# Optimization experiments

Hardware: AMD Instinct MI355X
Metric: run time of the kernel (lower is better)

## Reference

```python
import jax, jax.numpy as jnp
import numpy as np

NUM_HEADS = 8


def _mha(x, w_in, b_in, w_out, b_out, nh=NUM_HEADS):
    # x: [B, L, H]; torch nn.MultiheadAttention (batch_first) self-attention
    B, L, H = x.shape
    dh = H // nh
    qkv = x @ w_in.T + b_in                      # [B, L, 3H]
    q, k, v = jnp.split(qkv, 3, axis=-1)
    def heads(t):
        return t.reshape(B, L, nh, dh).transpose(0, 2, 1, 3)  # [B, nh, L, dh]
    q, k, v = heads(q), heads(k), heads(v)
    scale = 1.0 / np.sqrt(dh)
    scores = jnp.einsum('bhqd,bhkd->bhqk', q * scale, k)      # [B, nh, L, L]
    attn = jax.nn.softmax(scores, axis=-1)
    out = jnp.einsum('bhqk,bhkd->bhqd', attn, v)               # [B, nh, L, dh]
    out = out.transpose(0, 2, 1, 3).reshape(B, L, H)
    return out @ w_out.T + b_out


def setup_inputs() -> dict:
    key = jax.random.key(0)
    ks = jax.random.split(key, 10)
    S, M, B, H = 64, 4, 128, 1024
    std = 0.02
    inp = {
        'hidden_states_combined': jax.random.normal(ks[0], (S, M, B, 1, H), jnp.float32),
        'mf_in_w': jax.random.normal(ks[1], (3 * H, H), jnp.float32) * std,
        'mf_in_b': jnp.zeros((3 * H,), jnp.float32),
        'mf_out_w': jax.random.normal(ks[2], (H, H), jnp.float32) * std,
        'mf_out_b': jnp.zeros((H,), jnp.float32),
        'sf_in_w': jax.random.normal(ks[3], (3 * H, H), jnp.float32) * std,
        'sf_in_b': jnp.zeros((3 * H,), jnp.float32),
        'sf_out_w': jax.random.normal(ks[4], (H, H), jnp.float32) * std,
        'sf_out_b': jnp.zeros((H,), jnp.float32),
        'pos_enc': jax.random.normal(ks[5], (1, S, H), jnp.float32) * std,
    }
    return inp


def reference(hidden_states_combined, mf_in_w, mf_in_b, mf_out_w, mf_out_b,
              sf_in_w, sf_in_b, sf_out_w, sf_out_b, pos_enc):
    S, M, B, _, H = hidden_states_combined.shape
    # [S, M, B, 1, H] -> [S, B, M, H] -> batch all steps together: [S*B, M, H]
    x = hidden_states_combined[:, :, :, 0, :].transpose(0, 2, 1, 3).reshape(S * B, M, H)
    fused = _mha(x, mf_in_w, mf_in_b, mf_out_w, mf_out_b)        # [S*B, M, H]
    fused = fused.mean(axis=1).reshape(S, B, H)                  # mean over models
    seq = fused.transpose(1, 0, 2) + pos_enc[:, :S, :]            # [B, S, H]
    enhanced = _mha(seq, sf_in_w, sf_in_b, sf_out_w, sf_out_b)   # [B, S, H]
    return enhanced.transpose(1, 0, 2)[:, :, None, :]             # [S, B, 1, H]
```

## Files before the change

### kernel.cpp

```cpp
#include <hip/hip_runtime.h>

typedef unsigned short u16;
typedef __attribute__((ext_vector_type(8))) short bf16x8;
typedef __attribute__((ext_vector_type(4))) float f32x4;

__device__ __forceinline__ u16 f2bf(float f) {
  unsigned u = __float_as_uint(f);
  u += 0x7FFFu + ((u >> 16) & 1u);
  return (u16)(u >> 16);
}
__device__ __forceinline__ float bf2f(u16 h) {
  return __uint_as_float(((unsigned)h) << 16);
}

#define GLOAD16(g, l) __builtin_amdgcn_global_load_lds( \
    (const __attribute__((address_space(1))) void*)(g), \
    (__attribute__((address_space(3))) void*)(l), 16, 0, 0)

__global__ __launch_bounds__(256) void cvtw_kernel(const float* __restrict__ in,
                                                   u16* __restrict__ out, int n4) {
  int i = blockIdx.x * 256 + threadIdx.x;
  if (i >= n4) return;
  float4 f = ((const float4*)in)[i];
  ushort4 u;
  u.x = f2bf(f.x); u.y = f2bf(f.y); u.z = f2bf(f.z); u.w = f2bf(f.w);
  ((ushort4*)out)[i] = u;
}

__global__ __launch_bounds__(256) void xcvt_kernel(const float* __restrict__ hidden,
                                                   u16* __restrict__ xb, int s0) {
  int idx = blockIdx.x * 256 + threadIdx.x;
  int h4 = idx & 255;
  int lrow = idx >> 8;
  int m = lrow & 3;
  int b = (lrow >> 2) & 127;
  int sl = lrow >> 9;
  int s = s0 + sl;
  const float4 f = *(const float4*)(hidden + (((size_t)(s * 4 + m) * 128 + b) * 1024) + h4 * 4);
  ushort4 u;
  u.x = f2bf(f.x); u.y = f2bf(f.y); u.z = f2bf(f.z); u.w = f2bf(f.w);
  *(ushort4*)(xb + (size_t)lrow * 1024 + h4 * 4) = u;
}

template <int MODE>
__global__ __launch_bounds__(256) void gemm_bt(const u16* __restrict__ A,
                                               const u16* __restrict__ Bw,
                                               const float* __restrict__ bias,
                                               void* __restrict__ Cout,
                                               int M, int N, int K,
                                               const float* __restrict__ posenc) {
  __shared__ u16 As[128 * 32];
  __shared__ u16 Bs[128 * 32];
  const int t = threadIdx.x;
  const int w = t >> 6, l = t & 63;
  const int rowBase = blockIdx.y * 128, colBase = blockIdx.x * 128;
  const int wr = (w >> 1) * 64, wc = (w & 1) * 64;
  const int lr = l & 15, lg = l >> 4;
  const int sl = (lg ^ (lr & 3)) * 8;

  const int r0 = t >> 2,         s0 = (((t) & 3) ^ (r0 & 3)) * 8;
  const int r1 = (t + 256) >> 2, s1 = (((t + 256) & 3) ^ (r1 & 3)) * 8;
  const u16* A0 = A + (size_t)(rowBase + r0) * K + s0;
  const u16* A1 = A + (size_t)(rowBase + r1) * K + s1;
  const u16* B0 = Bw + (size_t)(colBase + r0) * K + s0;
  const u16* B1 = Bw + (size_t)(colBase + r1) * K + s1;
  u16* lA0 = As + (w * 64) * 8;
  u16* lA1 = As + (256 + w * 64) * 8;
  u16* lB0 = Bs + (w * 64) * 8;
  u16* lB1 = Bs + (256 + w * 64) * 8;

  f32x4 acc[4][4];
#pragma unroll
  for (int i = 0; i < 4; i++)
#pragma unroll
    for (int j = 0; j < 4; j++) acc[i][j] = (f32x4){0.f, 0.f, 0.f, 0.f};

  for (int k0 = 0; k0 < K; k0 += 32) {
    GLOAD16(A0 + k0, lA0);
    GLOAD16(A1 + k0, lA1);
    GLOAD16(B0 + k0, lB0);
    GLOAD16(B1 + k0, lB1);
    __syncthreads();
    bf16x8 af[4], bfv[4];
#pragma unroll
    for (int i = 0; i < 4; i++) af[i] = *(const bf16x8*)(As + (wr + i * 16 + lr) * 32 + sl);
#pragma unroll
    for (int j = 0; j < 4; j++) bfv[j] = *(const bf16x8*)(Bs + (wc + j * 16 + lr) * 32 + sl);
#pragma unroll
    for (int i = 0; i < 4; i++)
#pragma unroll
      for (int j = 0; j < 4; j++)
        acc[i][j] = __builtin_amdgcn_mfma_f32_16x16x32_bf16(af[i], bfv[j], acc[i][j], 0, 0, 0);
    __syncthreads();
  }

  const int orow0 = rowBase + wr + lg * 4;
  const int ocol0 = colBase + wc + lr;
#pragma unroll
  for (int i = 0; i < 4; i++) {
#pragma unroll
    for (int j = 0; j < 4; j++) {
#pragma unroll
      for (int r = 0; r < 4; r++) {
        int row = orow0 + i * 16 + r;
        int col = ocol0 + j * 16;
        float v = acc[i][j][r] + bias[col];
        if (MODE == 0) {
          ((u16*)Cout)[(size_t)row * N + col] = f2bf(v);
        } else if (MODE == 1) {
          int s = row >> 7, b = row & 127;
          v += posenc[s * 1024 + col];
          ((u16*)Cout)[((size_t)(b * 64 + s)) * 1024 + col] = f2bf(v);
        } else {
          int s = row & 63, b = row >> 6;
          ((float*)Cout)[((size_t)(s * 128 + b)) * 1024 + col] = v;
        }
      }
    }
  }
}

__global__ __launch_bounds__(256) void attn1_kernel(const u16* __restrict__ qkv,
                                                    u16* __restrict__ am, int seqBase) {
  const int w = threadIdx.x >> 6, l = threadIdx.x & 63;
  const int pair = blockIdx.x * 4 + w;
  const int seq = pair >> 3, head = pair & 7;
  const int d0 = l * 2;
  const u16* base = qkv + (size_t)(seq * 4) * 3072 + head * 128 + d0;
  const float scale = 0.08838834764831845f;
  float q[4][2], k[4][2], v[4][2];
#pragma unroll
  for (int m = 0; m < 4; m++) {
    ushort2 uq = *(const ushort2*)(base + (size_t)m * 3072);
    ushort2 uk = *(const ushort2*)(base + (size_t)m * 3072 + 1024);
    ushort2 uv = *(const ushort2*)(base + (size_t)m * 3072 + 2048);
    q[m][0] = bf2f(uq.x) * scale; q[m][1] = bf2f(uq.y) * scale;
    k[m][0] = bf2f(uk.x);         k[m][1] = bf2f(uk.y);
    v[m][0] = bf2f(uv.x);         v[m][1] = bf2f(uv.y);
  }
  float sc[4][4];
#pragma unroll
  for (int i = 0; i < 4; i++)
#pragma unroll
    for (int j = 0; j < 4; j++)
      sc[i][j] = q[i][0] * k[j][0] + q[i][1] * k[j][1];
#pragma unroll
  for (int off = 32; off >= 1; off >>= 1)
#pragma unroll
    for (int i = 0; i < 4; i++)
#pragma unroll
      for (int j = 0; j < 4; j++)
        sc[i][j] += __shfl_xor(sc[i][j], off, 64);
  float pbar[4] = {0.f, 0.f, 0.f, 0.f};
#pragma unroll
  for (int i = 0; i < 4; i++) {
    float mx = fmaxf(fmaxf(sc[i][0], sc[i][1]), fmaxf(sc[i][2], sc[i][3]));
    float e0 = __expf(sc[i][0] - mx), e1 = __expf(sc[i][1] - mx);
    float e2 = __expf(sc[i][2] - mx), e3 = __expf(sc[i][3] - mx);
    float inv = 0.25f / (e0 + e1 + e2 + e3);
    pbar[0] += e0 * inv; pbar[1] += e1 * inv; pbar[2] += e2 * inv; pbar[3] += e3 * inv;
  }
  float o0 = pbar[0] * v[0][0] + pbar[1] * v[1][0] + pbar[2] * v[2][0] + pbar[3] * v[3][0];
  float o1 = pbar[0] * v[0][1] + pbar[1] * v[1][1] + pbar[2] * v[2][1] + pbar[3] * v[3][1];
  ushort2 ou; ou.x = f2bf(o0); ou.y = f2bf(o1);
  *(ushort2*)(am + (size_t)(seqBase + seq) * 1024 + head * 128 + d0) = ou;
}

__global__ __launch_bounds__(256) void attn2_kernel(const u16* __restrict__ qkv2,
                                                    u16* __restrict__ aout) {
  __shared__ u16 Qs[64 * 128];
  __shared__ u16 Ks[64 * 128];
  __shared__ u16 Vt[128 * 72];
  __shared__ u16 Ps[64 * 72];
  const int t = threadIdx.x, w = t >> 6, l = t & 63;
  const int lr = l & 15, lg = l >> 4;
  const int b = blockIdx.x >> 3, head = blockIdx.x & 7;
  const u16* qb = qkv2 + (size_t)(b * 64) * 3072 + head * 128;

#pragma unroll
  for (int c = 0; c < 4; c++) {
    int flat = c * 256 + t;
    int row = flat >> 4, sp = flat & 15;
    int sg = (sp ^ (row & 7)) * 8;
    GLOAD16(qb + (size_t)row * 3072 + sg, Qs + (c * 256 + w * 64) * 8);
    GLOAD16(qb + 1024 + (size_t)row * 3072 + sg, Ks + (c * 256 + w * 64) * 8);
  }
  const int dd = (t & 63) * 2, kb = t >> 6;
#pragma unroll
  for (int c = 0; c < 16; c++) {
    int k = c * 4 + kb;
    ushort2 vv = *(const ushort2*)(qb + 2048 + (size_t)k * 3072 + dd);
    Vt[(size_t)dd * 72 + k] = vv.x;
    Vt[(size_t)(dd + 1) * 72 + k] = vv.y;
  }
  __syncthreads();

  f32x4 sc[4];
#pragma unroll
  for (int cb = 0; cb < 4; cb++) sc[cb] = (f32x4){0.f, 0.f, 0.f, 0.f};
#pragma unroll
  for (int ks = 0; ks < 4; ks++) {
    bf16x8 aq = *(const bf16x8*)(Qs + (w * 16 + lr) * 128 + ((ks * 4 + lg) ^ (lr & 7)) * 8);
#pragma unroll
    for (int cb = 0; cb < 4; cb++) {
      bf16x8 bk = *(const bf16x8*)(Ks + (cb * 16 + lr) * 128 + ((ks * 4 + lg) ^ (lr & 7)) * 8);
      sc[cb] = __builtin_amdgcn_mfma_f32_16x16x32_bf16(aq, bk, sc[cb], 0, 0, 0);
    }
  }

  const float scale = 0.08838834764831845f;
#pragma unroll
  for (int r = 0; r < 4; r++) {
#pragma unroll
    for (int cb = 0; cb < 4; cb++) sc[cb][r] *= scale;
    float mx = fmaxf(fmaxf(sc[0][r], sc[1][r]), fmaxf(sc[2][r], sc[3][r]));
#pragma unroll
    for (int off = 1; off < 16; off <<= 1) mx = fmaxf(mx, __shfl_xor(mx, off, 64));
    float sum = 0.f;
#pragma unroll
    for (int cb = 0; cb < 4; cb++) {
      float e = __expf(sc[cb][r] - mx);
      sum += e;
      sc[cb][r] = e;
    }
#pragma unroll
    for (int off = 1; off < 16; off <<= 1) sum += __shfl_xor(sum, off, 64);
    float inv = 1.f / sum;
    int prow = w * 16 + lg * 4 + r;
#pragma unroll
    for (int cb = 0; cb < 4; cb++)
      Ps[(size_t)prow * 72 + cb * 16 + lr] = f2bf(sc[cb][r] * inv);
  }

  f32x4 o[8];
#pragma unroll
  for (int cb = 0; cb < 8; cb++) o[cb] = (f32x4){0.f, 0.f, 0.f, 0.f};
#pragma unroll
  for (int ks = 0; ks < 2; ks++) {
    bf16x8 ap = *(const bf16x8*)(Ps + (w * 16 + lr) * 72 + ks * 32 + lg * 8);
#pragma unroll
    for (int cb = 0; cb < 8; cb++) {
      bf16x8 bv = *(const bf16x8*)(Vt + (cb * 16 + lr) * 72 + ks * 32 + lg * 8);
      o[cb] = __builtin_amdgcn_mfma_f32_16x16x32_bf16(ap, bv, o[cb], 0, 0, 0);
    }
  }
#pragma unroll
  for (int cb = 0; cb < 8; cb++) {
#pragma unroll
    for (int r = 0; r < 4; r++) {
      int srow = w * 16 + lg * 4 + r;
      int d = cb * 16 + lr;
      aout[(size_t)(b * 64 + srow) * 1024 + head * 128 + d] = f2bf(o[cb][r]);
    }
  }
}

extern "C" void kernel_launch(void* const* d_in, const int* in_sizes, int n_in,
                              void* d_out, int out_size, void* d_ws, size_t ws_size,
                              hipStream_t stream) {
  const float* hidden   = (const float*)d_in[0];
  const float* mf_in_w  = (const float*)d_in[1];
  const float* mf_in_b  = (const float*)d_in[2];
  const float* mf_out_w = (const float*)d_in[3];
  const float* mf_out_b = (const float*)d_in[4];
  const float* sf_in_w  = (const float*)d_in[5];
  const float* sf_in_b  = (const float*)d_in[6];
  const float* sf_out_w = (const float*)d_in[7];
  const float* sf_out_b = (const float*)d_in[8];
  const float* pos_enc  = (const float*)d_in[9];

  char* ws = (char*)d_ws;
  u16* w_mf_in  = (u16*)(ws);
  u16* w_mf_out = (u16*)(ws + 6291456);
  u16* w_sf_in  = (u16*)(ws + 8388608);
  u16* w_sf_out = (u16*)(ws + 14680064);
  u16* xchunk   = (u16*)(ws + 16777216);
  u16* qkvbuf   = (u16*)(ws + 33554432);
  u16* attnmean = (u16*)(ws + 83886080);
  u16* seqbuf   = (u16*)(ws + 100663296);
  u16* a2out    = (u16*)(ws + 117440512);

  cvtw_kernel<<<3072, 256, 0, stream>>>(mf_in_w, w_mf_in, 786432);
  cvtw_kernel<<<1024, 256, 0, stream>>>(mf_out_w, w_mf_out, 262144);
  cvtw_kernel<<<3072, 256, 0, stream>>>(sf_in_w, w_sf_in, 786432);
  cvtw_kernel<<<1024, 256, 0, stream>>>(sf_out_w, w_sf_out, 262144);

  for (int c = 0; c < 4; ++c) {
    xcvt_kernel<<<8192, 256, 0, stream>>>(hidden, xchunk, c * 16);
    gemm_bt<0><<<dim3(24, 64), 256, 0, stream>>>(xchunk, w_mf_in, mf_in_b, qkvbuf,
                                                 8192, 3072, 1024, nullptr);
    attn1_kernel<<<4096, 256, 0, stream>>>(qkvbuf, attnmean, c * 2048);
  }

  gemm_bt<1><<<dim3(8, 64), 256, 0, stream>>>(attnmean, w_mf_out, mf_out_b, seqbuf,
                                              8192, 1024, 1024, pos_enc);
  gemm_bt<0><<<dim3(24, 64), 256, 0, stream>>>(seqbuf, w_sf_in, sf_in_b, qkvbuf,
                                               8192, 3072, 1024, nullptr);
  attn2_kernel<<<1024, 256, 0, stream>>>(qkvbuf, a2out);
  gemm_bt<2><<<dim3(8, 64), 256, 0, stream>>>(a2out, w_sf_out, sf_out_b, d_out,
                                              8192, 1024, 1024, nullptr);
}
```

Baseline: 573.8 us.

## Add 256x256 triple-buffered bf16 GEMM for QKV in-projections

Adds a new GEMM kernel with 256x256 output tiles, 512 threads, and a three-stage LDS ring fed by async global-to-LDS loads. It uses explicit vmcnt waits so the loads for tile k+2 overlap the MFMA work on tile k, and it raises wave priority around the MFMA block. Both in-projection GEMMs (8192x3072x1024) now use it. The larger tile gives more reuse per loaded byte, at the cost of higher register and LDS pressure (96KB LDS, 128 accumulator floats per lane) and a grid of only 384 blocks.

```diff
diff --git a/kernel.cpp b/kernel.cpp
--- a/kernel.cpp
+++ b/kernel.cpp
@@ -40,6 +40,95 @@
   ushort4 u;
   u.x = f2bf(f.x); u.y = f2bf(f.y); u.z = f2bf(f.z); u.w = f2bf(f.w);
   *(ushort4*)(xb + (size_t)lrow * 1024 + h4 * 4) = u;
+}
+
+__global__ __launch_bounds__(512, 2) void gemm256(const u16* __restrict__ A,
+                                                  const u16* __restrict__ Bw,
+                                                  const float* __restrict__ bias,
+                                                  u16* __restrict__ C,
+                                                  int N, int K) {
+  __shared__ u16 SA[3][8192];
+  __shared__ u16 SB[3][8192];
+  const int t = threadIdx.x, w = t >> 6, l = t & 63;
+  const int lr = l & 15, lg = l >> 4;
+  const int wm = w >> 2, wn = w & 3;
+  const int rowBase = blockIdx.y * 256, colBase = blockIdx.x * 256;
+
+  const int srow = l >> 2;
+  const int gsl = ((l & 3) ^ (srow & 3)) * 8;
+  const u16* Ag0 = A + (size_t)(rowBase + w * 16 + srow) * K + gsl;
+  const u16* Ag1 = Ag0 + (size_t)128 * K;
+  const u16* Bg0 = Bw + (size_t)(colBase + w * 16 + srow) * K + gsl;
+  const u16* Bg1 = Bg0 + (size_t)128 * K;
+
+  const int fsl = (lg ^ (lr & 3)) * 8;
+  const int aoffB = (wm * 128 + lr) * 32 + fsl;
+  const int boffB = (wn * 64 + lr) * 32 + fsl;
+
+  f32x4 acc[8][4];
+#pragma unroll
+  for (int i = 0; i < 8; i++)
+#pragma unroll
+    for (int j = 0; j < 4; j++) acc[i][j] = (f32x4){0.f, 0.f, 0.f, 0.f};
+
+#define STG(tt, bb) do { \
+    const int k0_ = (tt) * 32; \
+    GLOAD16(Ag0 + k0_, &SA[bb][w * 512]); \
+    GLOAD16(Ag1 + k0_, &SA[bb][4096 + w * 512]); \
+    GLOAD16(Bg0 + k0_, &SB[bb][w * 512]); \
+    GLOAD16(Bg1 + k0_, &SB[bb][4096 + w * 512]); \
+  } while (0)
+
+  const int nt = K >> 5;
+  STG(0, 0);
+  STG(1, 1);
+  asm volatile("s_waitcnt vmcnt(4)" ::: "memory");
+  __builtin_amdgcn_s_barrier();
+  asm volatile("" ::: "memory");
+
+  int b0 = 0, b1 = 1, b2 = 2;
+  for (int tile = 0; tile < nt; ++tile) {
+    if (tile + 2 < nt) STG(tile + 2, b2);
+    const u16* pa = SA[b0];
+    const u16* pb = SB[b0];
+    bf16x8 af[8], bfr[4];
+#pragma unroll
+    for (int i = 0; i < 8; i++) af[i] = *(const bf16x8*)(pa + aoffB + i * 512);
+#pragma unroll
+    for (int j = 0; j < 4; j++) bfr[j] = *(const bf16x8*)(pb + boffB + j * 512);
+    __builtin_amdgcn_s_setprio(1);
+#pragma unroll
+    for (int i = 0; i < 8; i++)
+#pragma unroll
+      for (int j = 0; j < 4; j++)
+        acc[i][j] = __builtin_amdgcn_mfma_f32_16x16x32_bf16(af[i], bfr[j], acc[i][j], 0, 0, 0);
+    __builtin_amdgcn_s_setprio(0);
+    if (tile + 2 < nt) {
+      asm volatile("s_waitcnt vmcnt(4)" ::: "memory");
+    } else {
+      asm volatile("s_waitcnt vmcnt(0)" ::: "memory");
+    }
+    __builtin_amdgcn_s_barrier();
+    asm volatile("" ::: "memory");
+    const int tmp = b0; b0 = b1; b1 = b2; b2 = tmp;
+  }
+#undef STG
+
+  const int orow0 = rowBase + wm * 128 + lg * 4;
+  const int ocol0 = colBase + wn * 64 + lr;
+#pragma unroll
+  for (int i = 0; i < 8; i++) {
+#pragma unroll
+    for (int j = 0; j < 4; j++) {
+      const int col = ocol0 + j * 16;
+      const float bv = bias[col];
+#pragma unroll
+      for (int r = 0; r < 4; r++) {
+        const int row = orow0 + i * 16 + r;
+        C[(size_t)row * N + col] = f2bf(acc[i][j][r] + bv);
+      }
+    }
+  }
 }
 
 template <int MODE>
@@ -105,9 +194,7 @@
         int row = orow0 + i * 16 + r;
         int col = ocol0 + j * 16;
         float v = acc[i][j][r] + bias[col];
-        if (MODE == 0) {
-          ((u16*)Cout)[(size_t)row * N + col] = f2bf(v);
-        } else if (MODE == 1) {
+        if (MODE == 1) {
           int s = row >> 7, b = row & 127;
           v += posenc[s * 1024 + col];
           ((u16*)Cout)[((size_t)(b * 64 + s)) * 1024 + col] = f2bf(v);
@@ -287,15 +374,15 @@
 
   for (int c = 0; c < 4; ++c) {
     xcvt_kernel<<<8192, 256, 0, stream>>>(hidden, xchunk, c * 16);
-    gemm_bt<0><<<dim3(24, 64), 256, 0, stream>>>(xchunk, w_mf_in, mf_in_b, qkvbuf,
-                                                 8192, 3072, 1024, nullptr);
+    gemm256<<<dim3(12, 32), 512, 0, stream>>>(xchunk, w_mf_in, mf_in_b, qkvbuf,
+                                              3072, 1024);
     attn1_kernel<<<4096, 256, 0, stream>>>(qkvbuf, attnmean, c * 2048);
   }
 
   gemm_bt<1><<<dim3(8, 64), 256, 0, stream>>>(attnmean, w_mf_out, mf_out_b, seqbuf,
                                               8192, 1024, 1024, pos_enc);
-  gemm_bt<0><<<dim3(24, 64), 256, 0, stream>>>(seqbuf, w_sf_in, sf_in_b, qkvbuf,
-                                               8192, 3072, 1024, nullptr);
+  gemm256<<<dim3(12, 32), 512, 0, stream>>>(seqbuf, w_sf_in, sf_in_b, qkvbuf,
+                                            3072, 1024);
   attn2_kernel<<<1024, 256, 0, stream>>>(qkvbuf, a2out);
   gemm_bt<2><<<dim3(8, 64), 256, 0, stream>>>(a2out, w_sf_out, sf_out_b, d_out,
                                               8192, 1024, 1024, nullptr);
```

New measurement: 640.6 us. 1.12x slower.

## Replace GEMM with triple-buffered 256x128 tile pipeline and block swizzle

Applied to the files above, without the earlier changes.

Replaces the single-buffered 128x128 bf16 GEMM with a 256x128 tile kernel that uses three LDS stages. Global-to-LDS loads for tile k+2 are issued while MFMAs run on tile k, using split load phases, explicit waitcnt, barriers and setprio. A block-index remap groups neighbouring tiles to improve L2 reuse. This removes the per-iteration load/sync stalls of the old kernel, at the cost of more LDS (72KB), more registers and a grid half as large.

```diff
diff --git a/kernel.cpp b/kernel.cpp
--- a/kernel.cpp
+++ b/kernel.cpp
@@ -43,68 +43,120 @@
 }
 
 template <int MODE>
-__global__ __launch_bounds__(256) void gemm_bt(const u16* __restrict__ A,
-                                               const u16* __restrict__ Bw,
-                                               const float* __restrict__ bias,
-                                               void* __restrict__ Cout,
-                                               int M, int N, int K,
-                                               const float* __restrict__ posenc) {
-  __shared__ u16 As[128 * 32];
-  __shared__ u16 Bs[128 * 32];
-  const int t = threadIdx.x;
-  const int w = t >> 6, l = t & 63;
-  const int rowBase = blockIdx.y * 128, colBase = blockIdx.x * 128;
-  const int wr = (w >> 1) * 64, wc = (w & 1) * 64;
+__global__ __launch_bounds__(256, 2) void gemm_fp(const u16* __restrict__ A,
+                                                  const u16* __restrict__ Bw,
+                                                  const float* __restrict__ bias,
+                                                  void* __restrict__ Cout,
+                                                  int N, int K,
+                                                  const float* __restrict__ posenc) {
+  __shared__ u16 SA[3][8192];
+  __shared__ u16 SB[3][4096];
+  const int t = threadIdx.x, w = t >> 6, l = t & 63;
   const int lr = l & 15, lg = l >> 4;
-  const int sl = (lg ^ (lr & 3)) * 8;
-
-  const int r0 = t >> 2,         s0 = (((t) & 3) ^ (r0 & 3)) * 8;
-  const int r1 = (t + 256) >> 2, s1 = (((t + 256) & 3) ^ (r1 & 3)) * 8;
-  const u16* A0 = A + (size_t)(rowBase + r0) * K + s0;
-  const u16* A1 = A + (size_t)(rowBase + r1) * K + s1;
-  const u16* B0 = Bw + (size_t)(colBase + r0) * K + s0;
-  const u16* B1 = Bw + (size_t)(colBase + r1) * K + s1;
-  u16* lA0 = As + (w * 64) * 8;
-  u16* lA1 = As + (256 + w * 64) * 8;
-  u16* lB0 = Bs + (w * 64) * 8;
-  u16* lB1 = Bs + (256 + w * 64) * 8;
-
-  f32x4 acc[4][4];
-#pragma unroll
-  for (int i = 0; i < 4; i++)
+  const int wm = w >> 1, wn = w & 1;
+
+  const int gx = gridDim.x;
+  const int nb = gx * gridDim.y;
+  const int id = blockIdx.y * gx + blockIdx.x;
+  const int id2 = (id & 7) * (nb >> 3) + (id >> 3);
+  const int rowBase = (id2 / gx) * 256, colBase = (id2 % gx) * 128;
+
+  const int srow = l >> 2;
+  const int ssl = ((l & 3) ^ (srow & 3)) * 8;
+  const u16* Ag = A + (size_t)(rowBase + w * 16 + srow) * K + ssl;
+  const u16* Bg = Bw + (size_t)(colBase + w * 16 + srow) * K + ssl;
+  u16* const lA = &SA[0][0] + w * 512;
+  u16* const lB = &SB[0][0] + w * 512;
+
+  const int fsw = (lg ^ (lr & 3)) * 8;
+  const int aoff = (wm * 128 + lr) * 32 + fsw;
+  const int boff = (wn * 64 + lr) * 32 + fsw;
+
+  f32x4 acc[8][4];
+#pragma unroll
+  for (int i = 0; i < 8; i++)
 #pragma unroll
     for (int j = 0; j < 4; j++) acc[i][j] = (f32x4){0.f, 0.f, 0.f, 0.f};
 
-  for (int k0 = 0; k0 < K; k0 += 32) {
-    GLOAD16(A0 + k0, lA0);
-    GLOAD16(A1 + k0, lA1);
-    GLOAD16(B0 + k0, lB0);
-    GLOAD16(B1 + k0, lB1);
-    __syncthreads();
-    bf16x8 af[4], bfv[4];
-#pragma unroll
-    for (int i = 0; i < 4; i++) af[i] = *(const bf16x8*)(As + (wr + i * 16 + lr) * 32 + sl);
-#pragma unroll
-    for (int j = 0; j < 4; j++) bfv[j] = *(const bf16x8*)(Bs + (wc + j * 16 + lr) * 32 + sl);
-#pragma unroll
-    for (int i = 0; i < 4; i++)
-#pragma unroll
-      for (int j = 0; j < 4; j++)
-        acc[i][j] = __builtin_amdgcn_mfma_f32_16x16x32_bf16(af[i], bfv[j], acc[i][j], 0, 0, 0);
-    __syncthreads();
-  }
-
-  const int orow0 = rowBase + wr + lg * 4;
-  const int ocol0 = colBase + wc + lr;
-#pragma unroll
-  for (int i = 0; i < 4; i++) {
-#pragma unroll
-    for (int j = 0; j < 4; j++) {
+#define STG_P0(tt, bb) do { \
+    const size_t ko_ = (size_t)(tt) * 32; \
+    GLOAD16(Ag + ko_,                    lA + (bb) * 8192); \
+    GLOAD16(Ag + ko_ + (size_t)64 * K,   lA + (bb) * 8192 + 2048); \
+    GLOAD16(Ag + ko_ + (size_t)128 * K,  lA + (bb) * 8192 + 4096); \
+  } while (0)
+#define STG_P1(tt, bb) do { \
+    const size_t ko_ = (size_t)(tt) * 32; \
+    GLOAD16(Ag + ko_ + (size_t)192 * K,  lA + (bb) * 8192 + 6144); \
+    GLOAD16(Bg + ko_,                    lB + (bb) * 4096); \
+    GLOAD16(Bg + ko_ + (size_t)64 * K,   lB + (bb) * 4096 + 2048); \
+  } while (0)
+
+  const int nt = K >> 5;
+  STG_P0(0, 0); STG_P1(0, 0);
+  STG_P0(1, 1); STG_P1(1, 1);
+  asm volatile("s_waitcnt vmcnt(6)" ::: "memory");
+  __builtin_amdgcn_s_barrier();
+
+  int bcur = 0;
+  for (int tt = 0; tt < nt; ++tt) {
+    const u16* pa = &SA[bcur][0];
+    const u16* pb = &SB[bcur][0];
+    const int bnext = (bcur + 2 > 2) ? bcur - 1 : bcur + 2;
+    bf16x8 af[4], bfr[4];
+
+#pragma unroll
+    for (int m = 0; m < 4; m++) af[m] = *(const bf16x8*)(pa + aoff + m * 512);
+#pragma unroll
+    for (int n = 0; n < 4; n++) bfr[n] = *(const bf16x8*)(pb + boff + n * 512);
+    if (tt + 2 < nt) STG_P0(tt + 2, bnext);
+    __builtin_amdgcn_s_barrier();
+    asm volatile("s_waitcnt lgkmcnt(0)" ::: "memory");
+    __builtin_amdgcn_sched_barrier(0);
+    __builtin_amdgcn_s_setprio(1);
+#pragma unroll
+    for (int m = 0; m < 4; m++)
+#pragma unroll
+      for (int n = 0; n < 4; n++)
+        acc[m][n] = __builtin_amdgcn_mfma_f32_16x16x32_bf16(af[m], bfr[n], acc[m][n], 0, 0, 0);
+    __builtin_amdgcn_s_setprio(0);
+    __builtin_amdgcn_s_barrier();
+
+#pragma unroll
+    for (int m = 0; m < 4; m++) af[m] = *(const bf16x8*)(pa + aoff + (m + 4) * 512);
+    if (tt + 2 < nt) STG_P1(tt + 2, bnext);
+    __builtin_amdgcn_s_barrier();
+    asm volatile("s_waitcnt lgkmcnt(0)" ::: "memory");
+    __builtin_amdgcn_sched_barrier(0);
+    __builtin_amdgcn_s_setprio(1);
+#pragma unroll
+    for (int m = 0; m < 4; m++)
+#pragma unroll
+      for (int n = 0; n < 4; n++)
+        acc[m + 4][n] = __builtin_amdgcn_mfma_f32_16x16x32_bf16(af[m], bfr[n], acc[m + 4][n], 0, 0, 0);
+    __builtin_amdgcn_s_setprio(0);
+    if (tt + 2 < nt) {
+      asm volatile("s_waitcnt vmcnt(6)" ::: "memory");
+    } else if (tt + 1 < nt) {
+      asm volatile("s_waitcnt vmcnt(0)" ::: "memory");
+    }
+    __builtin_amdgcn_s_barrier();
+    bcur = (bcur + 1 > 2) ? 0 : bcur + 1;
+  }
+#undef STG_P0
+#undef STG_P1
+
+  const int orow0 = rowBase + wm * 128 + lg * 4;
+  const int ocol0 = colBase + wn * 64 + lr;
+#pragma unroll
+  for (int m = 0; m < 8; m++) {
+#pragma unroll
+    for (int n = 0; n < 4; n++) {
+      const int col = ocol0 + n * 16;
+      const float bv = bias[col];
 #pragma unroll
       for (int r = 0; r < 4; r++) {
-        int row = orow0 + i * 16 + r;
-        int col = ocol0 + j * 16;
-        float v = acc[i][j][r] + bias[col];
+        const int row = orow0 + m * 16 + r;
+        float v = acc[m][n][r] + bv;
         if (MODE == 0) {
           ((u16*)Cout)[(size_t)row * N + col] = f2bf(v);
         } else if (MODE == 1) {
@@ -287,16 +339,16 @@
 
   for (int c = 0; c < 4; ++c) {
     xcvt_kernel<<<8192, 256, 0, stream>>>(hidden, xchunk, c * 16);
-    gemm_bt<0><<<dim3(24, 64), 256, 0, stream>>>(xchunk, w_mf_in, mf_in_b, qkvbuf,
-                                                 8192, 3072, 1024, nullptr);
+    gemm_fp<0><<<dim3(24, 32), 256, 0, stream>>>(xchunk, w_mf_in, mf_in_b, qkvbuf,
+                                                 3072, 1024, nullptr);
     attn1_kernel<<<4096, 256, 0, stream>>>(qkvbuf, attnmean, c * 2048);
   }
 
-  gemm_bt<1><<<dim3(8, 64), 256, 0, stream>>>(attnmean, w_mf_out, mf_out_b, seqbuf,
-                                              8192, 1024, 1024, pos_enc);
-  gemm_bt<0><<<dim3(24, 64), 256, 0, stream>>>(seqbuf, w_sf_in, sf_in_b, qkvbuf,
-                                               8192, 3072, 1024, nullptr);
+  gemm_fp<1><<<dim3(8, 32), 256, 0, stream>>>(attnmean, w_mf_out, mf_out_b, seqbuf,
+                                              1024, 1024, pos_enc);
+  gemm_fp<0><<<dim3(24, 32), 256, 0, stream>>>(seqbuf, w_sf_in, sf_in_b, qkvbuf,
+                                               3072, 1024, nullptr);
   attn2_kernel<<<1024, 256, 0, stream>>>(qkvbuf, a2out);
-  gemm_bt<2><<<dim3(8, 64), 256, 0, stream>>>(a2out, w_sf_out, sf_out_b, d_out,
-                                              8192, 1024, 1024, nullptr);
-}
+  gemm_fp<2><<<dim3(8, 32), 256, 0, stream>>>(a2out, w_sf_out, sf_out_b, d_out,
+                                              1024, 1024, nullptr);
+}
```

Measured after the change: 530.2 us. -7.6%, faster.
